# Optimization experiments

Hardware: AMD Instinct MI355X
Metric: run time of the kernel (lower is better)

Reference implementation:

```python
import jax, jax.numpy as jnp
import numpy as np

K = 1.0        # Lorentz curvature parameter
SQRT_K = 1.0
B, E, T = 128, 64, 2048
F1, D, F2, NC = 16, 2, 32, 4


def linner(u, v):
    # Lorentz inner product <u,v>_L over the last axis (time component first)
    return -u[..., :1] * v[..., :1] + jnp.sum(u[..., 1:] * v[..., 1:], axis=-1, keepdims=True)


def add_time(space):
    # manifold.add_time / projx: time = sqrt(K + ||space||^2)
    t = jnp.sqrt(K + jnp.sum(space * space, axis=-1, keepdims=True))
    return jnp.concatenate([t, space], axis=-1)


def conv2d(x, w, padding, groups=1):
    return jax.lax.conv_general_dilated(
        x, w, window_strides=(1, 1), padding=padding,
        dimension_numbers=('NCHW', 'OIHW', 'NCHW'), feature_group_count=groups)


def bn2d(x, gamma, beta, eps=1e-3):
    # BatchNorm2d (training-mode batch statistics, eps=0.001)
    mean = jnp.mean(x, axis=(0, 2, 3), keepdims=True)
    var = jnp.var(x, axis=(0, 2, 3), keepdims=True)
    return (x - mean) * jax.lax.rsqrt(var + eps) * gamma.reshape(1, -1, 1, 1) + beta.reshape(1, -1, 1, 1)


def avgpool_w(x, k=4):
    # torch AvgPool2d((1,k), stride=k), floor mode
    Wo = x.shape[-1] // k
    return jnp.mean(x[..., :Wo * k].reshape(x.shape[:-1] + (Wo, k)), axis=-1)


def lorentz_bn(x, s, eps=1e-5):
    # AdaMom-style Riemannian batch norm on the hyperboloid (eta=1 -> pure batch stats,
    # learn_mean=False -> target mean is origin, learn_std=True -> learnable scale s).
    C = x.shape[-1]
    o = jnp.zeros((C,), x.dtype).at[0].set(SQRT_K)                      # origin
    avg = jnp.mean(x, axis=0, keepdims=True)
    mu = SQRT_K * avg / jnp.sqrt(jnp.maximum(-linner(avg, avg), 1e-8))  # batch centroid
    xin = -linner(x, mu)                                                # >= K on manifold
    dist = SQRT_K * jnp.arccosh(jnp.maximum(xin / K, 1.0 + 1e-7))
    u = x - (xin / K) * mu                                              # log_mu direction
    v = dist * u / jnp.sqrt(jnp.maximum(linner(u, u), 1e-8))            # log_mu(x)
    var = jnp.mean(dist * dist, axis=0, keepdims=True)                  # scalar dispersion
    v = v + (linner(o, v) / (K - linner(mu, o))) * (mu + o)             # PT mu -> origin
    v = v * (s.reshape(1, 1, -1, 1) / jnp.sqrt(var + eps))
    n = jnp.sqrt(jnp.maximum(linner(v, v), 1e-9))
    return jnp.cosh(n / SQRT_K) * o + SQRT_K * jnp.sinh(n / SQRT_K) * v / n  # exp_origin


def lorentz_avgpool_w(x, k=4):
    # window mean followed by Lorentz centroid renormalization
    Bb, H, W, C = x.shape
    Wo = W // k
    avg = jnp.mean(x[:, :, :Wo * k, :].reshape(Bb, H, Wo, k, C), axis=3)
    return SQRT_K * avg / jnp.sqrt(jnp.maximum(-linner(avg, avg), 1e-8))


def lorentz_flatten(x):
    Bb, H, W, C = x.shape
    t = x[..., 0].reshape(Bb, -1)
    s = x[..., 1:].reshape(Bb, -1)
    t_new = jnp.sqrt(jnp.maximum(jnp.sum(t * t, axis=-1, keepdims=True) - (H * W - 1) * K, 1e-8))
    return jnp.concatenate([t_new, s], axis=-1)


def lorentz_mlr(x, a, z):
    inv = 1.0 / SQRT_K
    norm_z = jnp.linalg.norm(z, axis=-1)                                  # (NC,)
    w_t = jnp.sinh(inv * a) * norm_z
    beta = jnp.sqrt(jnp.maximum((jnp.cosh(inv * a) * norm_z) ** 2 - w_t ** 2, 1e-8))
    alpha = -x[:, :1] * w_t[None, :] + jnp.cosh(inv * a)[None, :] * (x[:, 1:] @ z.T)
    d = SQRT_K * jnp.abs(jnp.arcsinh(inv * alpha / beta[None, :]))
    return jnp.sign(alpha) * beta[None, :] * d


def setup_inputs():
    key = jax.random.key(0)
    ks = jax.random.split(key, 8)
    Cin = F1 * D + 1   # 33
    Cout = F2 + 1      # 33
    feat = F2 * 128    # flattened space dim: W 2049 -> 512 -> 513 -> 128
    return {
        'inputs': jax.random.normal(ks[0], (B, E, T), jnp.float32),
        'domains': jax.random.randint(ks[1], (B,), 0, 4, jnp.int32),
        'conv1_w': jax.random.normal(ks[2], (F1, 1, 1, 32), jnp.float32) / np.float32(np.sqrt(32.0)),
        'bn1_gamma': jnp.ones((F1,), jnp.float32),
        'bn1_beta': jnp.zeros((F1,), jnp.float32),
        'conv2_w': jax.random.normal(ks[3], (F1 * D, 1, E, 1), jnp.float32) / np.float32(np.sqrt(E)),
        'bn2_gamma': jnp.ones((F1 * D,), jnp.float32),
        'bn2_beta': jnp.zeros((F1 * D,), jnp.float32),
        'ec1_w': jax.random.normal(ks[4], (F1 * D, 1, 1, 16), jnp.float32) / np.float32(np.sqrt(16.0)),
        'lc1_w': jax.random.normal(ks[5], (Cout, Cin), jnp.float32) / np.float32(np.sqrt(Cin)),
        'bn_s': jnp.ones((513,), jnp.float32),
        'mlr_a': jax.random.normal(ks[6], (NC,), jnp.float32) * 0.01,
        'mlr_z': jax.random.normal(ks[7], (NC, feat), jnp.float32) * 0.01,
    }


def reference(inputs, domains, conv1_w, bn1_gamma, bn1_beta, conv2_w, bn2_gamma, bn2_beta,
              ec1_w, lc1_w, bn_s, mlr_a, mlr_z):
    x = inputs[:, None, :, :]                           # (B,1,E,T)
    x = conv2d(x, conv1_w, [(0, 0), (16, 16)])          # (B,16,64,2049)
    x = bn2d(x, bn1_gamma, bn1_beta)
    x = conv2d(x, conv2_w, [(0, 0), (0, 0)], groups=F1) # (B,32,1,2049) depthwise over electrodes
    x = bn2d(x, bn2_gamma, bn2_beta)
    x = jax.nn.elu(x)
    x = avgpool_w(x)                                    # (B,32,1,512)  (dropout = eval no-op)
    x = conv2d(x, ec1_w, [(0, 0), (8, 8)], groups=F1 * D)  # (B,32,1,513)
    x = jnp.transpose(x, (0, 2, 3, 1))                  # (B,1,513,32) channels-last
    x = x / (jnp.linalg.norm(x, axis=-1, keepdims=True) + 1e-8)
    x = add_time(x)                                     # projx(pad(x, (1,0))) -> (B,1,513,33)
    # LorentzConv2d 1x1 (kernel_len=1): clamp time, linear, recompute time from space output
    pre = jnp.concatenate([jnp.maximum(x[..., :1], SQRT_K), x[..., 1:]], axis=-1)
    y = jnp.einsum('bhwi,oi->bhwo', pre, lc1_w)
    x = add_time(y[..., 1:])
    x = lorentz_bn(x, bn_s)
    x = add_time(jax.nn.elu(x[..., 1:]))                # LorentzeLU
    x = lorentz_avgpool_w(x)                            # (B,1,128,33)
    feats = lorentz_flatten(x)                          # (B, 4097)
    logits = lorentz_mlr(feats, mlr_a, mlr_z)           # (B, 4)
    return logits, feats
```

## Files before the change

### kernel.cpp

```cpp
#include <hip/hip_runtime.h>
#include <math.h>

#define BB 128
#define EE 64
#define TT 2048
#define C2 32
#define W1 2049
#define WPW 512
#define FEAT 4096
#define NBLK 1024

#define OFF_P    ((size_t)0)
#define OFF_X2   ((size_t)4194304)
#define OFF_PSUM ((size_t)8388608)
#define OFF_PSQ  ((size_t)8421376)
#define OFF_SS   ((size_t)8454144)
#define OFF_H    ((size_t)8454208)
#define OFF_QSQ  ((size_t)10616896)

__device__ __forceinline__ unsigned short f2b(float f) {
    unsigned int u = __float_as_uint(f);
    u += 0x7FFFu + ((u >> 16) & 1u);
    return (unsigned short)(u >> 16);
}
__device__ __forceinline__ float b2f(unsigned short s) {
    return __uint_as_float(((unsigned int)s) << 16);
}

__global__ __launch_bounds__(256) void k_p(const float* __restrict__ in,
        const float* __restrict__ w2, unsigned short* __restrict__ P) {
    int b = blockIdx.y, t0 = blockIdx.x * 256, tid = threadIdx.x;
    __shared__ unsigned short li[64][256];
    __shared__ float lw2s[32][64];
    const float* ib = in + (size_t)b * EE * TT + t0;
    for (int j = tid; j < 64 * 64; j += 256) {
        int e = j >> 6, q = j & 63;
        float4 v = *(const float4*)(ib + e * TT + q * 4);
        li[e][q * 4 + 0] = f2b(v.x); li[e][q * 4 + 1] = f2b(v.y);
        li[e][q * 4 + 2] = f2b(v.z); li[e][q * 4 + 3] = f2b(v.w);
    }
    for (int j = tid; j < 2048; j += 256) lw2s[j >> 6][j & 63] = w2[j];
    __syncthreads();
    int cg = tid >> 6, colg = tid & 63;
    int c8 = cg * 8;
    float acc[4][8];
#pragma unroll
    for (int x = 0; x < 4; x++)
#pragma unroll
        for (int jj = 0; jj < 8; jj++) acc[x][jj] = 0.f;
    for (int e = 0; e < 64; e += 2) {
        uint2 r0 = *(const uint2*)&li[e][colg * 4];
        uint2 r1 = *(const uint2*)&li[e + 1][colg * 4];
        float v0[4], v1[4];
        v0[0] = __uint_as_float(r0.x << 16); v0[1] = __uint_as_float(r0.x & 0xFFFF0000u);
        v0[2] = __uint_as_float(r0.y << 16); v0[3] = __uint_as_float(r0.y & 0xFFFF0000u);
        v1[0] = __uint_as_float(r1.x << 16); v1[1] = __uint_as_float(r1.x & 0xFFFF0000u);
        v1[2] = __uint_as_float(r1.y << 16); v1[3] = __uint_as_float(r1.y & 0xFFFF0000u);
#pragma unroll
        for (int jj = 0; jj < 8; jj++) {
            float2 wv = *(const float2*)&lw2s[c8 + jj][e];
#pragma unroll
            for (int x = 0; x < 4; x++) {
                acc[x][jj] = fmaf(wv.x, v0[x], acc[x][jj]);
                acc[x][jj] = fmaf(wv.y, v1[x], acc[x][jj]);
            }
        }
    }
    unsigned short* Pb = P + (size_t)b * C2 * TT + t0 + colg * 4;
#pragma unroll
    for (int jj = 0; jj < 8; jj++) {
        int c = c8 + jj;
        uint2 o;
        o.x = (unsigned int)f2b(acc[0][jj]) | ((unsigned int)f2b(acc[1][jj]) << 16);
        o.y = (unsigned int)f2b(acc[2][jj]) | ((unsigned int)f2b(acc[3][jj]) << 16);
        *(uint2*)(Pb + (size_t)c * TT) = o;
    }
}

__global__ __launch_bounds__(256) void k_cs(const unsigned short* __restrict__ P,
        const float* __restrict__ w1, const float* __restrict__ g1,
        unsigned short* __restrict__ x2, float* __restrict__ psum, float* __restrict__ psq) {
    int bx = blockIdx.x, b = blockIdx.y, w0 = bx * 256, tid = threadIdx.x;
    __shared__ unsigned short lp[32][288];
    __shared__ float lw1[16][32];
    __shared__ float lds_s[32], lds_q[32];
    const unsigned short* Pb = P + (size_t)b * C2 * TT;
    for (int j = tid; j < 32 * 72; j += 256) {
        int c = j / 72, g4 = j % 72;
        int t = w0 - 16 + g4 * 4;
        uint2 v = make_uint2(0u, 0u);
        if (t >= 0 && t + 3 < TT) v = *(const uint2*)(Pb + (size_t)c * TT + t);
        *(uint2*)&lp[c][g4 * 4] = v;
    }
    for (int j = tid; j < 512; j += 256) {
        int g = j >> 5;
        float sgn = (g1[g] < 0.f) ? -1.f : 1.f;
        lw1[g][j & 31] = w1[j] * sgn;
    }
    __syncthreads();
    for (int r = 0; r < 8; r++) {
        int task = r * 256 + tid;
        int c = task >> 6;
        int wq = task & 63;
        int wbase = wq * 4;
        float win[36];
#pragma unroll
        for (int i = 0; i < 9; i++) {
            uint2 v = *(const uint2*)&lp[c][wbase + i * 4];
            win[i * 4 + 0] = __uint_as_float(v.x << 16);
            win[i * 4 + 1] = __uint_as_float(v.x & 0xFFFF0000u);
            win[i * 4 + 2] = __uint_as_float(v.y << 16);
            win[i * 4 + 3] = __uint_as_float(v.y & 0xFFFF0000u);
        }
        const float* wc = lw1[c >> 1];
        float ls = 0.f, lq = 0.f;
        float accs[4];
#pragma unroll
        for (int i = 0; i < 4; i++) {
            float acc = 0.f;
#pragma unroll
            for (int k = 0; k < 32; k++) acc = fmaf(wc[k], win[i + k], acc);
            accs[i] = acc;
            ls += acc; lq = fmaf(acc, acc, lq);
        }
        uint2 o;
        o.x = (unsigned int)f2b(accs[0]) | ((unsigned int)f2b(accs[1]) << 16);
        o.y = (unsigned int)f2b(accs[2]) | ((unsigned int)f2b(accs[3]) << 16);
        *(uint2*)(x2 + ((size_t)b * C2 + c) * TT + w0 + wbase) = o;
#pragma unroll
        for (int d = 1; d < 64; d <<= 1) {
            ls += __shfl_xor(ls, d);
            lq += __shfl_xor(lq, d);
        }
        if ((tid & 63) == 0) { lds_s[c] = ls; lds_q[c] = lq; }
    }
    __syncthreads();
    if (bx == 7 && tid < 32) {
        const float* wc = lw1[tid >> 1];
        float acc = 0.f;
#pragma unroll
        for (int k = 0; k < 16; k++) acc = fmaf(wc[k], b2f(lp[tid][256 + k]), acc);
        lds_s[tid] += acc;
        lds_q[tid] += acc * acc;
    }
    __syncthreads();
    if (tid < 32) {
        int blk = b * 8 + bx;
        psum[tid * NBLK + blk] = lds_s[tid];
        psq[tid * NBLK + blk]  = lds_q[tid];
    }
}

__global__ __launch_bounds__(64) void k_bn2fin(
        const float* __restrict__ psum, const float* __restrict__ psq,
        const float* __restrict__ gamma, const float* __restrict__ beta,
        float* __restrict__ ss) {
    int c = blockIdx.x, l = threadIdx.x;
    float s = 0.f, q = 0.f;
    for (int j = l; j < NBLK; j += 64) { s += psum[c * NBLK + j]; q += psq[c * NBLK + j]; }
#pragma unroll
    for (int d = 1; d < 64; d <<= 1) { s += __shfl_xor(s, d); q += __shfl_xor(q, d); }
    if (l == 0) {
        float n = (float)(BB * W1);
        float m = s / n;
        float var = q / n - m * m;
        float sc = gamma[c] * rsqrtf(var + 1e-3f);
        ss[c] = sc;
        ss[32 + c] = beta[c] - m * sc;
    }
}

__global__ __launch_bounds__(256) void k_mid(
        const unsigned short* __restrict__ x2, const float* __restrict__ ss,
        const float* __restrict__ ew, const float* __restrict__ lc1,
        float* __restrict__ H) {
    int b = blockIdx.y, w0 = blockIdx.x * 64, tid = threadIdx.x;
    __shared__ unsigned short lx[32][324];
    __shared__ float ly[32][82];
    __shared__ float lss[64];
    __shared__ float lew[32][17];
    __shared__ float lc[1089];
    __shared__ float lxn[8][32];
    const unsigned short* xb = x2 + (size_t)b * C2 * TT;
    int base_t = 4 * w0 - 32;
    for (int it = 0; it < 10; it++) {
        int idx = it * 256 + tid;
        int c = idx / 80, q = idx - c * 80;
        int t0 = base_t + q * 4;
        uint2 v = make_uint2(0u, 0u);
        if (t0 >= 0 && t0 <= TT - 4) v = *(const uint2*)(xb + (size_t)c * TT + t0);
        *(uint2*)&lx[c][q * 4] = v;
    }
    if (tid < 64) lss[tid] = ss[tid];
    for (int j = tid; j < 512; j += 256) lew[j >> 4][j & 15] = ew[j];
    for (int j = tid; j < 1089; j += 256) lc[j] = lc1[j];
    __syncthreads();
    for (int it = 0; it < 10; it++) {
        int idx = it * 256 + tid;
        int c = idx & 31, j2 = idx >> 5;
        int ty = w0 - 8 + j2;
        float r = 0.f;
        if (ty >= 0 && ty < WPW) {
            uint2 v = *(const uint2*)&lx[c][j2 * 4];
            float sc = lss[c], sh = lss[32 + c];
            float a0 = fmaf(sc, __uint_as_float(v.x << 16), sh);
            float a1 = fmaf(sc, __uint_as_float(v.x & 0xFFFF0000u), sh);
            float a2 = fmaf(sc, __uint_as_float(v.y << 16), sh);
            float a3 = fmaf(sc, __uint_as_float(v.y & 0xFFFF0000u), sh);
            r = ((a0 > 0.f) ? a0 : expm1f(a0)) + ((a1 > 0.f) ? a1 : expm1f(a1))
              + ((a2 > 0.f) ? a2 : expm1f(a2)) + ((a3 > 0.f) ? a3 : expm1f(a3));
            r *= 0.25f;
        }
        ly[c][j2] = r;
    }
    __syncthreads();
    int c = tid & 31, wl = tid >> 5;
    float win[24];
#pragma unroll
    for (int m = 0; m < 12; m++) {
        float2 v = *(const float2*)&ly[c][wl * 8 + m * 2];
        win[m * 2] = v.x; win[m * 2 + 1] = v.y;
    }
    float wc[16];
#pragma unroll
    for (int k = 0; k < 16; k++) wc[k] = lew[c][k];
    float acc[8];
#pragma unroll
    for (int i = 0; i < 8; i++) {
        float a = 0.f;
#pragma unroll
        for (int k = 0; k < 16; k++) a = fmaf(wc[k], win[i + k], a);
        acc[i] = a;
    }
    float wt0 = lc[(c + 1) * 33];
    float wreg[32];
#pragma unroll
    for (int k = 0; k < 32; k++) wreg[k] = lc[(c + 1) * 33 + 1 + k];
    float* lrow = lxn[wl];
#pragma unroll 1
    for (int i = 0; i < 8; i++) {
        float v = acc[i];
        float ssq = v * v;
        ssq += __shfl_xor(ssq, 1);  ssq += __shfl_xor(ssq, 2);
        ssq += __shfl_xor(ssq, 4);  ssq += __shfl_xor(ssq, 8);
        ssq += __shfl_xor(ssq, 16);
        float inv = 1.f / (sqrtf(ssq) + 1e-8f);
        float xn = v * inv;
        float s2 = ssq * inv * inv;
        float pre0 = fmaxf(sqrtf(1.f + s2), 1.f);
        lrow[c] = xn;
        float y = wt0 * pre0;
#pragma unroll
        for (int q = 0; q < 8; q++) {
            float4 xv = *(const float4*)&lrow[q * 4];
            y = fmaf(wreg[q * 4 + 0], xv.x, y);
            y = fmaf(wreg[q * 4 + 1], xv.y, y);
            y = fmaf(wreg[q * 4 + 2], xv.z, y);
            y = fmaf(wreg[q * 4 + 3], xv.w, y);
        }
        float sy = y * y;
        sy += __shfl_xor(sy, 1);  sy += __shfl_xor(sy, 2);
        sy += __shfl_xor(sy, 4);  sy += __shfl_xor(sy, 8);
        sy += __shfl_xor(sy, 16);
        int w = w0 + wl * 8 + i;
        float* hrow = H + ((size_t)w * BB + b) * 33;
        hrow[1 + c] = y;
        if (c == 0) hrow[0] = sqrtf(1.f + sy);
    }
}

__global__ __launch_bounds__(512) void k_tail(
        const float* __restrict__ H, const float* __restrict__ bs,
        float* __restrict__ outp, float* __restrict__ qsq) {
    int wp = blockIdx.x;
    int tid = threadIdx.x;
    int j = tid >> 7;
    int b = tid & 127;
    int w = wp * 4 + j;
    __shared__ float wsum[4][2][33];
    __shared__ float vred[4][2];
    __shared__ float lavg[128][33];
    float* lz = &lavg[0][0];
    for (int i = tid; i < 128 * 33; i += 512) lz[i] = 0.f;
    float x[33];
    const float* hp = H + ((size_t)w * BB + b) * 33;
#pragma unroll
    for (int ch = 0; ch < 33; ch++) x[ch] = hp[ch];
    float mu[33];
#pragma unroll
    for (int ch = 0; ch < 33; ch++) {
        float s = x[ch];
        s += __shfl_xor(s, 1);  s += __shfl_xor(s, 2);  s += __shfl_xor(s, 4);
        s += __shfl_xor(s, 8);  s += __shfl_xor(s, 16); s += __shfl_xor(s, 32);
        mu[ch] = s;
    }
    int wv = b >> 6;
    if ((b & 63) == 0) {
#pragma unroll
        for (int ch = 0; ch < 33; ch++) wsum[j][wv][ch] = mu[ch];
    }
    __syncthreads();
#pragma unroll
    for (int ch = 0; ch < 33; ch++) mu[ch] = (wsum[j][0][ch] + wsum[j][1][ch]) * (1.f / 128.f);
    float a0 = mu[0], sp = 0.f;
#pragma unroll
    for (int i = 1; i < 33; i++) sp = fmaf(mu[i], mu[i], sp);
    float rd = rsqrtf(fmaxf(a0 * a0 - sp, 1e-8f));
#pragma unroll
    for (int ch = 0; ch < 33; ch++) mu[ch] *= rd;
    float xin2 = x[0] * mu[0];
#pragma unroll
    for (int i = 1; i < 33; i++) xin2 -= x[i] * mu[i];
    float dist = acoshf(fmaxf(xin2, 1.f + 1e-7f));
    float dq = dist * dist;
    dq += __shfl_xor(dq, 1);  dq += __shfl_xor(dq, 2);  dq += __shfl_xor(dq, 4);
    dq += __shfl_xor(dq, 8);  dq += __shfl_xor(dq, 16); dq += __shfl_xor(dq, 32);
    if ((b & 63) == 0) vred[j][wv] = dq;
    __syncthreads();
    float var = (vred[j][0] + vred[j][1]) * (1.f / 128.f);
#pragma unroll
    for (int ch = 0; ch < 33; ch++) x[ch] = x[ch] - xin2 * mu[ch];
    float lu = -x[0] * x[0];
#pragma unroll
    for (int i = 1; i < 33; i++) lu = fmaf(x[i], x[i], lu);
    float f = dist * rsqrtf(fmaxf(lu, 1e-8f));
#pragma unroll
    for (int ch = 0; ch < 33; ch++) x[ch] *= f;
    float corr = -x[0] / (1.f + mu[0]);
    x[0] += corr * (mu[0] + 1.f);
#pragma unroll
    for (int i = 1; i < 33; i++) x[i] = fmaf(corr, mu[i], x[i]);
    float scb = bs[w] * rsqrtf(var + 1e-5f);
#pragma unroll
    for (int ch = 0; ch < 33; ch++) x[ch] *= scb;
    float nn = -x[0] * x[0];
#pragma unroll
    for (int i = 1; i < 33; i++) nn = fmaf(x[i], x[i], nn);
    float n = sqrtf(fmaxf(nn, 1e-9f));
    float shn = sinhf(n) / n;
    float sg = 0.f;
#pragma unroll
    for (int i = 1; i < 33; i++) {
        float e = shn * x[i];
        e = (e > 0.f) ? e : expm1f(e);
        x[i] = e;
        sg = fmaf(e, e, sg);
    }
    x[0] = sqrtf(1.f + sg);
    for (int jj = 0; jj < 4; jj++) {
        if (j == jj) {
#pragma unroll
            for (int ch = 0; ch < 33; ch++) lavg[b][ch] += x[ch];
        }
        __syncthreads();
    }
    if (tid < 128) {
        int bb2 = tid;
        float avg[33];
#pragma unroll
        for (int ch = 0; ch < 33; ch++) avg[ch] = lavg[bb2][ch] * 0.25f;
        float sp2 = 0.f;
#pragma unroll
        for (int i = 1; i < 33; i++) sp2 = fmaf(avg[i], avg[i], sp2);
        float l = avg[0] * avg[0] - sp2;
        float rd2 = rsqrtf(fmaxf(l, 1e-8f));
        float q0 = avg[0] * rd2;
        float* fb = outp + 512 + (size_t)bb2 * 4097;
#pragma unroll
        for (int i = 1; i < 33; i++) fb[1 + wp * 32 + (i - 1)] = avg[i] * rd2;
        qsq[bb2 * 128 + wp] = q0 * q0;
    }
}

__global__ __launch_bounds__(256) void k_mlr2(
        const float* __restrict__ qsq, const float* __restrict__ z,
        const float* __restrict__ a, float* __restrict__ outp) {
    int b = blockIdx.x, tid = threadIdx.x;
    __shared__ float red[4][8];
    __shared__ float tnsh;
    if (tid < 64) {
        float s = qsq[b * 128 + tid] + qsq[b * 128 + 64 + tid];
#pragma unroll
        for (int d = 1; d < 64; d <<= 1) s += __shfl_xor(s, d);
        if (tid == 0) tnsh = sqrtf(fmaxf(s - 127.f, 1e-8f));
    }
    __syncthreads();
    float tn = tnsh;
    const float* fs = outp + 512 + (size_t)b * 4097 + 1;
    float sdot[4] = {0.f, 0.f, 0.f, 0.f}, sq[4] = {0.f, 0.f, 0.f, 0.f};
    for (int i = tid * 4; i < FEAT; i += 1024) {
        float f0 = fs[i], f1 = fs[i + 1], f2 = fs[i + 2], f3 = fs[i + 3];
#pragma unroll
        for (int c = 0; c < 4; c++) {
            float4 zv = *(const float4*)(z + c * FEAT + i);
            sdot[c] = fmaf(f0, zv.x, sdot[c]); sdot[c] = fmaf(f1, zv.y, sdot[c]);
            sdot[c] = fmaf(f2, zv.z, sdot[c]); sdot[c] = fmaf(f3, zv.w, sdot[c]);
            sq[c] = fmaf(zv.x, zv.x, sq[c]); sq[c] = fmaf(zv.y, zv.y, sq[c]);
            sq[c] = fmaf(zv.z, zv.z, sq[c]); sq[c] = fmaf(zv.w, zv.w, sq[c]);
        }
    }
#pragma unroll
    for (int d = 1; d < 64; d <<= 1) {
#pragma unroll
        for (int c = 0; c < 4; c++) {
            sdot[c] += __shfl_xor(sdot[c], d);
            sq[c]   += __shfl_xor(sq[c], d);
        }
    }
    int wv = tid >> 6;
    if ((tid & 63) == 0) {
#pragma unroll
        for (int c = 0; c < 4; c++) { red[wv][c] = sdot[c]; red[wv][4 + c] = sq[c]; }
    }
    __syncthreads();
    if (tid == 0) {
        outp[512 + (size_t)b * 4097] = tn;
#pragma unroll
        for (int c = 0; c < 4; c++) {
            float dot = red[0][c] + red[1][c] + red[2][c] + red[3][c];
            float qz  = red[0][4 + c] + red[1][4 + c] + red[2][4 + c] + red[3][4 + c];
            float nz = sqrtf(qz);
            float ca = coshf(a[c]), sa = sinhf(a[c]);
            float wt = sa * nz;
            float cb = ca * nz;
            float bb = sqrtf(fmaxf(cb * cb - wt * wt, 1e-8f));
            float alpha = fmaf(-tn, wt, ca * dot);
            float d = fabsf(asinhf(alpha / bb));
            float sg = (alpha > 0.f) ? 1.f : ((alpha < 0.f) ? -1.f : 0.f);
            outp[b * 4 + c] = sg * bb * d;
        }
    }
}

extern "C" void kernel_launch(void* const* d_in, const int* in_sizes, int n_in,
                              void* d_out, int out_size, void* d_ws, size_t ws_size,
                              hipStream_t stream) {
    const float* in   = (const float*)d_in[0];
    const float* w1   = (const float*)d_in[2];
    const float* g1   = (const float*)d_in[3];
    const float* w2   = (const float*)d_in[5];
    const float* g2   = (const float*)d_in[6];
    const float* b2   = (const float*)d_in[7];
    const float* ew   = (const float*)d_in[8];
    const float* lc1  = (const float*)d_in[9];
    const float* bs   = (const float*)d_in[10];
    const float* mlra = (const float*)d_in[11];
    const float* mlrz = (const float*)d_in[12];
    float* out = (float*)d_out;
    float* ws = (float*)d_ws;

    unsigned short* P  = (unsigned short*)(ws + OFF_P);
    unsigned short* X2 = (unsigned short*)(ws + OFF_X2);
    float* PSUM = ws + OFF_PSUM;
    float* PSQ  = ws + OFF_PSQ;
    float* SS   = ws + OFF_SS;
    float* H    = ws + OFF_H;
    float* QSQ  = ws + OFF_QSQ;

    k_p<<<dim3(8, 128), 256, 0, stream>>>(in, w2, P);
    k_cs<<<dim3(8, 128), 256, 0, stream>>>(P, w1, g1, X2, PSUM, PSQ);
    k_bn2fin<<<32, 64, 0, stream>>>(PSUM, PSQ, g2, b2, SS);
    k_mid<<<dim3(8, 128), 256, 0, stream>>>(X2, SS, ew, lc1, H);
    k_tail<<<128, 512, 0, stream>>>(H, bs, out, QSQ);
    k_mlr2<<<128, 256, 0, stream>>>(QSQ, mlrz, mlra, out);
}
```

Before: 203.6 us.

## Split Lorentz BN tail into per-position kernel and pooling kernel, batch shuffles in mid

The old single tail kernel, run on 128 blocks with 33 channels per thread, becomes two kernels. k_tail2 runs 512 blocks, one per width position, with two lanes per batch row each holding half the channels, and writes the post-ELU manifold points to a new workspace buffer G. k_pool then averages groups of four positions and writes the features. k_mid now reads the bf16 input straight from global memory instead of staging it in shared memory, batches its eight row reductions so the shuffles interleave, reads the lc1 weights from global memory, and uses __expf for ELU. The aim is more parallelism and fewer serialized shuffles, at the cost of an extra kernel launch, an extra round trip through memory for G, and a slightly less accurate ELU.

Result: no change. 202.2 us (-0.7%).

```diff
diff --git a/kernel.cpp b/kernel.cpp
--- a/kernel.cpp
+++ b/kernel.cpp
@@ -17,6 +17,7 @@
 #define OFF_SS   ((size_t)8454144)
 #define OFF_H    ((size_t)8454208)
 #define OFF_QSQ  ((size_t)10616896)
+#define OFF_G    ((size_t)10633280)
 
 __device__ __forceinline__ unsigned short f2b(float f) {
     unsigned int u = __float_as_uint(f);
@@ -25,6 +26,9 @@
 }
 __device__ __forceinline__ float b2f(unsigned short s) {
     return __uint_as_float(((unsigned int)s) << 16);
+}
+__device__ __forceinline__ float elu_fast(float a) {
+    return (a > 0.f) ? a : (__expf(a) - 1.f);
 }
 
 __global__ __launch_bounds__(256) void k_p(const float* __restrict__ in,
@@ -175,43 +179,29 @@
         const float* __restrict__ ew, const float* __restrict__ lc1,
         float* __restrict__ H) {
     int b = blockIdx.y, w0 = blockIdx.x * 64, tid = threadIdx.x;
-    __shared__ unsigned short lx[32][324];
-    __shared__ float ly[32][82];
+    __shared__ __align__(16) float ly[32][82];
     __shared__ float lss[64];
     __shared__ float lew[32][17];
-    __shared__ float lc[1089];
-    __shared__ float lxn[8][32];
+    __shared__ __align__(16) float lxn[8][8][32];
+    if (tid < 64) lss[tid] = ss[tid];
+    for (int j = tid; j < 512; j += 256) lew[j >> 4][j & 15] = ew[j];
+    __syncthreads();
     const unsigned short* xb = x2 + (size_t)b * C2 * TT;
-    int base_t = 4 * w0 - 32;
     for (int it = 0; it < 10; it++) {
         int idx = it * 256 + tid;
         int c = idx / 80, q = idx - c * 80;
-        int t0 = base_t + q * 4;
-        uint2 v = make_uint2(0u, 0u);
-        if (t0 >= 0 && t0 <= TT - 4) v = *(const uint2*)(xb + (size_t)c * TT + t0);
-        *(uint2*)&lx[c][q * 4] = v;
-    }
-    if (tid < 64) lss[tid] = ss[tid];
-    for (int j = tid; j < 512; j += 256) lew[j >> 4][j & 15] = ew[j];
-    for (int j = tid; j < 1089; j += 256) lc[j] = lc1[j];
-    __syncthreads();
-    for (int it = 0; it < 10; it++) {
-        int idx = it * 256 + tid;
-        int c = idx & 31, j2 = idx >> 5;
-        int ty = w0 - 8 + j2;
+        int ty = w0 - 8 + q;
         float r = 0.f;
         if (ty >= 0 && ty < WPW) {
-            uint2 v = *(const uint2*)&lx[c][j2 * 4];
+            uint2 v = *(const uint2*)(xb + (size_t)c * TT + ty * 4);
             float sc = lss[c], sh = lss[32 + c];
-            float a0 = fmaf(sc, __uint_as_float(v.x << 16), sh);
-            float a1 = fmaf(sc, __uint_as_float(v.x & 0xFFFF0000u), sh);
-            float a2 = fmaf(sc, __uint_as_float(v.y << 16), sh);
-            float a3 = fmaf(sc, __uint_as_float(v.y & 0xFFFF0000u), sh);
-            r = ((a0 > 0.f) ? a0 : expm1f(a0)) + ((a1 > 0.f) ? a1 : expm1f(a1))
-              + ((a2 > 0.f) ? a2 : expm1f(a2)) + ((a3 > 0.f) ? a3 : expm1f(a3));
-            r *= 0.25f;
-        }
-        ly[c][j2] = r;
+            float a0 = elu_fast(fmaf(sc, __uint_as_float(v.x << 16), sh));
+            float a1 = elu_fast(fmaf(sc, __uint_as_float(v.x & 0xFFFF0000u), sh));
+            float a2 = elu_fast(fmaf(sc, __uint_as_float(v.y << 16), sh));
+            float a3 = elu_fast(fmaf(sc, __uint_as_float(v.y & 0xFFFF0000u), sh));
+            r = (a0 + a1 + a2 + a3) * 0.25f;
+        }
+        ly[c][q] = r;
     }
     __syncthreads();
     int c = tid & 31, wl = tid >> 5;
@@ -232,144 +222,182 @@
         for (int k = 0; k < 16; k++) a = fmaf(wc[k], win[i + k], a);
         acc[i] = a;
     }
-    float wt0 = lc[(c + 1) * 33];
+    float ss8[8];
+#pragma unroll
+    for (int i = 0; i < 8; i++) ss8[i] = acc[i] * acc[i];
+#pragma unroll
+    for (int d = 1; d < 32; d <<= 1) {
+#pragma unroll
+        for (int i = 0; i < 8; i++) ss8[i] += __shfl_xor(ss8[i], d);
+    }
+    float pre0[8];
+#pragma unroll
+    for (int i = 0; i < 8; i++) {
+        float inv = 1.f / (sqrtf(ss8[i]) + 1e-8f);
+        lxn[wl][i][c] = acc[i] * inv;
+        float s2 = ss8[i] * inv * inv;
+        pre0[i] = fmaxf(sqrtf(1.f + s2), 1.f);
+    }
+    float wt0 = lc1[(c + 1) * 33];
     float wreg[32];
 #pragma unroll
-    for (int k = 0; k < 32; k++) wreg[k] = lc[(c + 1) * 33 + 1 + k];
-    float* lrow = lxn[wl];
-#pragma unroll 1
+    for (int k = 0; k < 32; k++) wreg[k] = lc1[(c + 1) * 33 + 1 + k];
+    float y8[8];
+#pragma unroll
     for (int i = 0; i < 8; i++) {
-        float v = acc[i];
-        float ssq = v * v;
-        ssq += __shfl_xor(ssq, 1);  ssq += __shfl_xor(ssq, 2);
-        ssq += __shfl_xor(ssq, 4);  ssq += __shfl_xor(ssq, 8);
-        ssq += __shfl_xor(ssq, 16);
-        float inv = 1.f / (sqrtf(ssq) + 1e-8f);
-        float xn = v * inv;
-        float s2 = ssq * inv * inv;
-        float pre0 = fmaxf(sqrtf(1.f + s2), 1.f);
-        lrow[c] = xn;
-        float y = wt0 * pre0;
+        float y = wt0 * pre0[i];
 #pragma unroll
         for (int q = 0; q < 8; q++) {
-            float4 xv = *(const float4*)&lrow[q * 4];
+            float4 xv = *(const float4*)&lxn[wl][i][q * 4];
             y = fmaf(wreg[q * 4 + 0], xv.x, y);
             y = fmaf(wreg[q * 4 + 1], xv.y, y);
             y = fmaf(wreg[q * 4 + 2], xv.z, y);
             y = fmaf(wreg[q * 4 + 3], xv.w, y);
         }
-        float sy = y * y;
-        sy += __shfl_xor(sy, 1);  sy += __shfl_xor(sy, 2);
-        sy += __shfl_xor(sy, 4);  sy += __shfl_xor(sy, 8);
-        sy += __shfl_xor(sy, 16);
+        y8[i] = y;
+    }
+    float sy8[8];
+#pragma unroll
+    for (int i = 0; i < 8; i++) sy8[i] = y8[i] * y8[i];
+#pragma unroll
+    for (int d = 1; d < 32; d <<= 1) {
+#pragma unroll
+        for (int i = 0; i < 8; i++) sy8[i] += __shfl_xor(sy8[i], d);
+    }
+#pragma unroll
+    for (int i = 0; i < 8; i++) {
         int w = w0 + wl * 8 + i;
         float* hrow = H + ((size_t)w * BB + b) * 33;
-        hrow[1 + c] = y;
-        if (c == 0) hrow[0] = sqrtf(1.f + sy);
-    }
-}
-
-__global__ __launch_bounds__(512) void k_tail(
+        hrow[1 + c] = y8[i];
+        if (c == 0) hrow[0] = sqrtf(1.f + sy8[i]);
+    }
+}
+
+__global__ __launch_bounds__(256) void k_tail2(
         const float* __restrict__ H, const float* __restrict__ bs,
-        float* __restrict__ outp, float* __restrict__ qsq) {
-    int wp = blockIdx.x;
+        float* __restrict__ G) {
+    int w = blockIdx.x;
     int tid = threadIdx.x;
-    int j = tid >> 7;
-    int b = tid & 127;
-    int w = wp * 4 + j;
-    __shared__ float wsum[4][2][33];
-    __shared__ float vred[4][2];
-    __shared__ float lavg[128][33];
-    float* lz = &lavg[0][0];
-    for (int i = tid; i < 128 * 33; i += 512) lz[i] = 0.f;
-    float x[33];
+    int l = tid & 1, b = tid >> 1;
+    int wv = tid >> 6;
+    __shared__ float wsum[4][2][17];
+    __shared__ float vsum[4];
+    float x[17];
     const float* hp = H + ((size_t)w * BB + b) * 33;
 #pragma unroll
-    for (int ch = 0; ch < 33; ch++) x[ch] = hp[ch];
-    float mu[33];
-#pragma unroll
-    for (int ch = 0; ch < 33; ch++) {
-        float s = x[ch];
-        s += __shfl_xor(s, 1);  s += __shfl_xor(s, 2);  s += __shfl_xor(s, 4);
-        s += __shfl_xor(s, 8);  s += __shfl_xor(s, 16); s += __shfl_xor(s, 32);
-        mu[ch] = s;
-    }
-    int wv = b >> 6;
-    if ((b & 63) == 0) {
-#pragma unroll
-        for (int ch = 0; ch < 33; ch++) wsum[j][wv][ch] = mu[ch];
-    }
-    __syncthreads();
-#pragma unroll
-    for (int ch = 0; ch < 33; ch++) mu[ch] = (wsum[j][0][ch] + wsum[j][1][ch]) * (1.f / 128.f);
-    float a0 = mu[0], sp = 0.f;
-#pragma unroll
-    for (int i = 1; i < 33; i++) sp = fmaf(mu[i], mu[i], sp);
-    float rd = rsqrtf(fmaxf(a0 * a0 - sp, 1e-8f));
-#pragma unroll
-    for (int ch = 0; ch < 33; ch++) mu[ch] *= rd;
-    float xin2 = x[0] * mu[0];
-#pragma unroll
-    for (int i = 1; i < 33; i++) xin2 -= x[i] * mu[i];
-    float dist = acoshf(fmaxf(xin2, 1.f + 1e-7f));
+    for (int k = 0; k < 17; k++) {
+        int ch = 2 * k + l;
+        x[k] = (ch < 33) ? hp[ch] : 0.f;
+    }
+    float mu[17];
+#pragma unroll
+    for (int k = 0; k < 17; k++) mu[k] = x[k];
+#pragma unroll
+    for (int d = 2; d < 64; d <<= 1) {
+#pragma unroll
+        for (int k = 0; k < 17; k++) mu[k] += __shfl_xor(mu[k], d);
+    }
+    if ((tid & 63) < 2) {
+#pragma unroll
+        for (int k = 0; k < 17; k++) wsum[wv][tid & 1][k] = mu[k];
+    }
+    __syncthreads();
+#pragma unroll
+    for (int k = 0; k < 17; k++)
+        mu[k] = (wsum[0][l][k] + wsum[1][l][k] + wsum[2][l][k] + wsum[3][l][k]) * (1.f / 128.f);
+    float a0 = (l == 0) ? mu[0] : 0.f;
+    a0 += __shfl_xor(a0, 1);
+    float spp = 0.f;
+#pragma unroll
+    for (int k = 0; k < 17; k++) spp = fmaf(mu[k], mu[k], spp);
+    if (l == 0) spp -= 2.f * mu[0] * mu[0];
+    spp += __shfl_xor(spp, 1);
+    float rd = rsqrtf(fmaxf(-spp, 1e-8f));
+#pragma unroll
+    for (int k = 0; k < 17; k++) mu[k] *= rd;
+    float mu0 = a0 * rd;
+    float pp = 0.f;
+#pragma unroll
+    for (int k = 0; k < 17; k++) pp = fmaf(x[k], mu[k], pp);
+    if (l == 0) pp -= 2.f * x[0] * mu[0];
+    pp += __shfl_xor(pp, 1);
+    float xin = -pp;
+    float dist = acoshf(fmaxf(xin, 1.f + 1e-7f));
     float dq = dist * dist;
-    dq += __shfl_xor(dq, 1);  dq += __shfl_xor(dq, 2);  dq += __shfl_xor(dq, 4);
-    dq += __shfl_xor(dq, 8);  dq += __shfl_xor(dq, 16); dq += __shfl_xor(dq, 32);
-    if ((b & 63) == 0) vred[j][wv] = dq;
-    __syncthreads();
-    float var = (vred[j][0] + vred[j][1]) * (1.f / 128.f);
-#pragma unroll
-    for (int ch = 0; ch < 33; ch++) x[ch] = x[ch] - xin2 * mu[ch];
-    float lu = -x[0] * x[0];
-#pragma unroll
-    for (int i = 1; i < 33; i++) lu = fmaf(x[i], x[i], lu);
-    float f = dist * rsqrtf(fmaxf(lu, 1e-8f));
-#pragma unroll
-    for (int ch = 0; ch < 33; ch++) x[ch] *= f;
-    float corr = -x[0] / (1.f + mu[0]);
-    x[0] += corr * (mu[0] + 1.f);
-#pragma unroll
-    for (int i = 1; i < 33; i++) x[i] = fmaf(corr, mu[i], x[i]);
+#pragma unroll
+    for (int d = 2; d < 64; d <<= 1) dq += __shfl_xor(dq, d);
+    if ((tid & 63) == 0) vsum[wv] = dq;
+    __syncthreads();
+    float var = (vsum[0] + vsum[1] + vsum[2] + vsum[3]) * (1.f / 128.f);
+#pragma unroll
+    for (int k = 0; k < 17; k++) x[k] = x[k] - xin * mu[k];
+    float lup = 0.f;
+#pragma unroll
+    for (int k = 0; k < 17; k++) lup = fmaf(x[k], x[k], lup);
+    if (l == 0) lup -= 2.f * x[0] * x[0];
+    lup += __shfl_xor(lup, 1);
+    float f = dist * rsqrtf(fmaxf(lup, 1e-8f));
+#pragma unroll
+    for (int k = 0; k < 17; k++) x[k] *= f;
+    float v0 = (l == 0) ? x[0] : 0.f;
+    v0 += __shfl_xor(v0, 1);
+    float corr = -v0 / (1.f + mu0);
+#pragma unroll
+    for (int k = 0; k < 17; k++) x[k] = fmaf(corr, mu[k], x[k]);
+    if (l == 0) x[0] += corr;
     float scb = bs[w] * rsqrtf(var + 1e-5f);
 #pragma unroll
-    for (int ch = 0; ch < 33; ch++) x[ch] *= scb;
-    float nn = -x[0] * x[0];
-#pragma unroll
-    for (int i = 1; i < 33; i++) nn = fmaf(x[i], x[i], nn);
-    float n = sqrtf(fmaxf(nn, 1e-9f));
+    for (int k = 0; k < 17; k++) x[k] *= scb;
+    float nnp = 0.f;
+#pragma unroll
+    for (int k = 0; k < 17; k++) nnp = fmaf(x[k], x[k], nnp);
+    if (l == 0) nnp -= 2.f * x[0] * x[0];
+    nnp += __shfl_xor(nnp, 1);
+    float n = sqrtf(fmaxf(nnp, 1e-9f));
     float shn = sinhf(n) / n;
-    float sg = 0.f;
-#pragma unroll
-    for (int i = 1; i < 33; i++) {
-        float e = shn * x[i];
-        e = (e > 0.f) ? e : expm1f(e);
-        x[i] = e;
-        sg = fmaf(e, e, sg);
-    }
-    x[0] = sqrtf(1.f + sg);
-    for (int jj = 0; jj < 4; jj++) {
-        if (j == jj) {
-#pragma unroll
-            for (int ch = 0; ch < 33; ch++) lavg[b][ch] += x[ch];
-        }
-        __syncthreads();
-    }
-    if (tid < 128) {
-        int bb2 = tid;
-        float avg[33];
-#pragma unroll
-        for (int ch = 0; ch < 33; ch++) avg[ch] = lavg[bb2][ch] * 0.25f;
-        float sp2 = 0.f;
-#pragma unroll
-        for (int i = 1; i < 33; i++) sp2 = fmaf(avg[i], avg[i], sp2);
-        float l = avg[0] * avg[0] - sp2;
-        float rd2 = rsqrtf(fmaxf(l, 1e-8f));
-        float q0 = avg[0] * rd2;
-        float* fb = outp + 512 + (size_t)bb2 * 4097;
-#pragma unroll
-        for (int i = 1; i < 33; i++) fb[1 + wp * 32 + (i - 1)] = avg[i] * rd2;
-        qsq[bb2 * 128 + wp] = q0 * q0;
-    }
+    float e[17];
+#pragma unroll
+    for (int k = 0; k < 17; k++) e[k] = elu_fast(shn * x[k]);
+    float sgp = 0.f;
+#pragma unroll
+    for (int k = 0; k < 17; k++) sgp = fmaf(e[k], e[k], sgp);
+    if (l == 0) sgp -= e[0] * e[0];
+    sgp += __shfl_xor(sgp, 1);
+    float g0 = sqrtf(1.f + sgp);
+    float* gp = G + ((size_t)w * BB + b) * 33;
+#pragma unroll
+    for (int k = 0; k < 17; k++) {
+        int ch = 2 * k + l;
+        if (ch >= 1 && ch < 33) gp[ch] = e[k];
+    }
+    if (l == 0) gp[0] = g0;
+}
+
+__global__ __launch_bounds__(256) void k_pool(
+        const float* __restrict__ G, float* __restrict__ outp,
+        float* __restrict__ qsq) {
+    int item = blockIdx.x * 256 + threadIdx.x;
+    int wp = item >> 7, b = item & 127;
+    float avg[33];
+#pragma unroll
+    for (int ch = 0; ch < 33; ch++) avg[ch] = 0.f;
+    for (int j = 0; j < 4; j++) {
+        const float* gp = G + ((size_t)(wp * 4 + j) * BB + b) * 33;
+#pragma unroll
+        for (int ch = 0; ch < 33; ch++) avg[ch] += gp[ch];
+    }
+#pragma unroll
+    for (int ch = 0; ch < 33; ch++) avg[ch] *= 0.25f;
+    float sp2 = 0.f;
+#pragma unroll
+    for (int i = 1; i < 33; i++) sp2 = fmaf(avg[i], avg[i], sp2);
+    float lnr = avg[0] * avg[0] - sp2;
+    float rd2 = rsqrtf(fmaxf(lnr, 1e-8f));
+    float q0 = avg[0] * rd2;
+    float* fb = outp + 512 + (size_t)b * 4097;
+#pragma unroll
+    for (int i = 1; i < 33; i++) fb[1 + wp * 32 + (i - 1)] = avg[i] * rd2;
+    qsq[b * 128 + wp] = q0 * q0;
 }
 
 __global__ __launch_bounds__(256) void k_mlr2(
@@ -456,11 +484,13 @@
     float* SS   = ws + OFF_SS;
     float* H    = ws + OFF_H;
     float* QSQ  = ws + OFF_QSQ;
+    float* G    = ws + OFF_G;
 
     k_p<<<dim3(8, 128), 256, 0, stream>>>(in, w2, P);
     k_cs<<<dim3(8, 128), 256, 0, stream>>>(P, w1, g1, X2, PSUM, PSQ);
     k_bn2fin<<<32, 64, 0, stream>>>(PSUM, PSQ, g2, b2, SS);
     k_mid<<<dim3(8, 128), 256, 0, stream>>>(X2, SS, ew, lc1, H);
-    k_tail<<<128, 512, 0, stream>>>(H, bs, out, QSQ);
+    k_tail2<<<512, 256, 0, stream>>>(H, bs, G);
+    k_pool<<<64, 256, 0, stream>>>(G, out, QSQ);
     k_mlr2<<<128, 256, 0, stream>>>(QSQ, mlrz, mlra, out);
 }
```
